# Optimization experiments

Hardware: AMD Instinct MI355X
Metric: run time of the kernel (lower is better)

Reference implementation:

```python
import jax, jax.numpy as jnp
import numpy as np

N, TX, NH, H, E, V = 64, 1024, 512, 512, 300, 32000
IP = NH + H            # attention input size = 1024
HALF = IP // 2         # 512
BN_EPS = 1e-5


def setup_inputs() -> dict:
    key = jax.random.key(0)
    ks = jax.random.split(key, 24)
    p = lambda k, shape: jax.random.normal(k, shape, dtype=jnp.float32) * 0.05
    embed_W = p(ks[0], (V, E)).at[0].set(0.0)  # padding_idx=0 row zeroed
    return {
        "yt_prev": jax.random.randint(ks[1], (N,), 0, V, dtype=jnp.int32),
        "h0": jax.random.normal(ks[2], (N, H), dtype=jnp.float32),
        "c0": jax.random.normal(ks[3], (N, H), dtype=jnp.float32),
        "h1": jax.random.normal(ks[4], (N, H), dtype=jnp.float32),
        "c1": jax.random.normal(ks[5], (N, H), dtype=jnp.float32),
        "encoder_output": jax.random.normal(ks[6], (N, TX, NH), dtype=jnp.float32),
        "c_prev": jax.random.normal(ks[7], (N, NH), dtype=jnp.float32),
        "embed_W": embed_W,
        # pre LSTM cell: input = NH + E
        "pre_W_ih": p(ks[8], (4 * H, NH + E)), "pre_W_hh": p(ks[9], (4 * H, H)),
        "pre_b_ih": p(ks[10], (4 * H,)), "pre_b_hh": p(ks[11], (4 * H,)),
        # post LSTM cell: input = H + NH
        "post_W_ih": p(ks[12], (4 * H, H + NH)), "post_W_hh": p(ks[13], (4 * H, H)),
        "post_b_ih": p(ks[14], (4 * H,)), "post_b_hh": p(ks[15], (4 * H,)),
        # attention MLP
        "att_W1": p(ks[16], (HALF, IP)), "att_b1": p(ks[17], (HALF,)),
        "att_W2": p(ks[18], (1, HALF)), "att_b2": p(ks[19], (1,)),
        # classifier
        "mlp_W": p(ks[20], (V, H)), "mlp_b": p(ks[21], (V,)),
        "bn_gamma": jnp.ones((V,), jnp.float32), "bn_beta": jnp.zeros((V,), jnp.float32),
    }


def _lstm_cell(x, h, c, W_ih, W_hh, b_ih, b_hh):
    # PyTorch LSTMCell gate order: i, f, g, o
    g = x @ W_ih.T + h @ W_hh.T + (b_ih + b_hh)
    i, f, gg, o = jnp.split(g, 4, axis=-1)
    c_new = jax.nn.sigmoid(f) * c + jax.nn.sigmoid(i) * jnp.tanh(gg)
    h_new = jax.nn.sigmoid(o) * jnp.tanh(c_new)
    return h_new, c_new


def reference(yt_prev, h0, c0, h1, c1, encoder_output, c_prev, embed_W,
              pre_W_ih, pre_W_hh, pre_b_ih, pre_b_hh,
              post_W_ih, post_W_hh, post_b_ih, post_b_hh,
              att_W1, att_b1, att_W2, att_b2,
              mlp_W, mlp_b, bn_gamma, bn_beta):
    # embedding lookup + concat with previous context
    y_emb = embed_W[yt_prev]                              # [N, E]
    rnn_input = jnp.concatenate([y_emb, c_prev], axis=1)  # [N, E+NH]
    h_0, c_0 = _lstm_cell(rnn_input, h0, c0, pre_W_ih, pre_W_hh, pre_b_ih, pre_b_hh)
    s_i = h_0
    # Bahdanau attention over encoder timesteps
    Tx = encoder_output.shape[1]
    s_exp = jnp.broadcast_to(s_i[:, None, :], (s_i.shape[0], Tx, s_i.shape[1]))
    concat = jnp.concatenate([encoder_output, s_exp], axis=2)  # [N, Tx, IP]
    e = jax.nn.relu(concat @ att_W1.T + att_b1)                # [N, Tx, HALF]
    scores = e @ att_W2.T + att_b2                             # [N, Tx, 1]
    alphas = jax.nn.softmax(scores, axis=1)                    # softmax over Tx
    context = jnp.sum(alphas * encoder_output, axis=1)         # [N, NH]
    # post LSTM cell
    spell_input = jnp.concatenate([s_i, context], axis=1)
    h_1, c_1 = _lstm_cell(spell_input, h1, c1, post_W_ih, post_W_hh, post_b_ih, post_b_hh)
    # classifier: linear -> relu -> batchnorm(train mode, batch stats) -> softmax
    z = jax.nn.relu(h_1 @ mlp_W.T + mlp_b)                     # [N, V]
    mean = jnp.mean(z, axis=0)
    var = jnp.mean((z - mean) ** 2, axis=0)                    # biased, as in PyTorch training
    z_bn = bn_gamma * (z - mean) * jax.lax.rsqrt(var + BN_EPS) + bn_beta
    out = jax.nn.softmax(z_bn, axis=1)
    return out, h_0, c_0, h_1, c_1, context
```

## Files before the change

### kernel.cpp

```cpp
#include <hip/hip_runtime.h>
#include <math.h>

#define DEVFN __device__ __forceinline__

typedef __attribute__((ext_vector_type(4))) float f32x4;
typedef __attribute__((ext_vector_type(8))) __bf16 bf16x8;
typedef __attribute__((ext_vector_type(8))) short short8v;

#define NB   64
#define TXD  1024
#define NHD  512
#define HSZ  512
#define ESZ  300
#define VSZ  32000
#define G4   (4*HSZ)
#define KPRE (ESZ + NHD + HSZ)
#define KPOST 1536
#define HALFD 512

DEVFN short f2bf(float f) {
  unsigned u = __float_as_uint(f);
  u = (u + 0x7fffu + ((u >> 16) & 1u)) >> 16;
  return (short)u;
}
DEVFN float sigm(float x) { return 1.0f / (1.0f + __expf(-x)); }

DEVFN short8v pack8(float4 a, float4 b) {
  short8v v;
  v[0]=f2bf(a.x); v[1]=f2bf(a.y); v[2]=f2bf(a.z); v[3]=f2bf(a.w);
  v[4]=f2bf(b.x); v[5]=f2bf(b.y); v[6]=f2bf(b.z); v[7]=f2bf(b.w);
  return v;
}
DEVFN void gload16(const void* g, void* lds_base) {
  __builtin_amdgcn_global_load_lds(
      (const __attribute__((address_space(1))) unsigned int*)g,
      (__attribute__((address_space(3))) unsigned int*)lds_base, 16, 0, 0);
}

DEVFN float4 ldA4(const float* __restrict__ A, int lda, int row, int k, int Ka) {
  if (k >= Ka) { float4 z = {0.f,0.f,0.f,0.f}; return z; }
  return *(const float4*)(A + (size_t)row * lda + k);
}
DEVFN float4 ldB4(const float* __restrict__ B1, int ldb1, int split,
                  const float* __restrict__ B2, int ldb2, int row, int k, int Ka) {
  if (k >= Ka) { float4 z = {0.f,0.f,0.f,0.f}; return z; }
  if (k < split) return *(const float4*)(B1 + (size_t)row * ldb1 + k);
  return *(const float4*)(B2 + (size_t)row * ldb2 + (k - split));
}

__global__ __launch_bounds__(256)
void prep(const int* __restrict__ yt, const float* __restrict__ embW,
          const float* __restrict__ c_prev, const float* __restrict__ h0,
          const float* __restrict__ W1, unsigned short* __restrict__ W1b,
          float* __restrict__ cat)
{
  int b = blockIdx.x;
  if (b < 128) {
    int i = b * 256 + threadIdx.x;
    int c = i >> 6, kq = (i & 63) * 8;
    float4 a = *(const float4*)(W1 + (size_t)c * 1024 + kq);
    float4 bb = *(const float4*)(W1 + (size_t)c * 1024 + kq + 4);
    *(short8v*)(W1b + (size_t)c * 512 + kq) = pack8(a, bb);
  } else {
    int i = (b - 128) * 256 + threadIdx.x;
    if (i >= NB * KPRE) return;
    int n = i / KPRE, c = i - n * KPRE;
    float v;
    if (c < ESZ)            v = embW[(size_t)yt[n] * ESZ + c];
    else if (c < ESZ + NHD) v = c_prev[(size_t)n * NHD + (c - ESZ)];
    else                    v = h0[(size_t)n * HSZ + (c - ESZ - NHD)];
    cat[i] = v;
  }
}

template<int EPI>
__global__ __launch_bounds__(256)
void mfma_gemm128(const float* __restrict__ A, int lda, int Ka,
                  const float* __restrict__ B1, int ldb1, int split,
                  const float* __restrict__ B2, int ldb2,
                  const float* __restrict__ bias1,
                  float* __restrict__ C, int ldc, int Kslice,
                  const float* __restrict__ gamma, const float* __restrict__ beta,
                  float* __restrict__ bnsc, float* __restrict__ bnsh)
{
  __shared__ __align__(16) short As[64][40];
  __shared__ __align__(16) short Bs[128][40];
  const int tid = threadIdx.x;
  const int w = tid >> 6, lane = tid & 63;
  const int wr = w >> 1, wc = w & 1;
  const int cl = lane & 15, g = lane >> 4;
  const int n0 = blockIdx.x * 128;
  const int ks = blockIdx.y;
  const int kbeg = ks * Kslice;
  const int kend = min(kbeg + Kslice, Ka);
  C += (size_t)ks * 64 * ldc;

  const f32x4 fz = {0.f,0.f,0.f,0.f};
  f32x4 acc[2][4];
  #pragma unroll
  for (int i = 0; i < 2; ++i)
    #pragma unroll
    for (int j = 0; j < 4; ++j) acc[i][j] = fz;

  const int sr  = tid >> 2;
  const int skc = (tid & 3) * 8;

  float4 ra0, ra1, rb0[2], rb1[2];
  ra0 = ldA4(A, lda, sr, kbeg + skc, Ka);
  ra1 = ldA4(A, lda, sr, kbeg + skc + 4, Ka);
  #pragma unroll
  for (int it = 0; it < 2; ++it) {
    rb0[it] = ldB4(B1, ldb1, split, B2, ldb2, n0 + sr + it*64, kbeg + skc, Ka);
    rb1[it] = ldB4(B1, ldb1, split, B2, ldb2, n0 + sr + it*64, kbeg + skc + 4, Ka);
  }

  for (int k0 = kbeg; k0 < kend; k0 += 32) {
    __syncthreads();
    *(short8v*)&As[sr][skc] = pack8(ra0, ra1);
    #pragma unroll
    for (int it = 0; it < 2; ++it)
      *(short8v*)&Bs[sr + it*64][skc] = pack8(rb0[it], rb1[it]);
    __syncthreads();
    if (k0 + 32 < kend) {
      ra0 = ldA4(A, lda, sr, k0 + 32 + skc, Ka);
      ra1 = ldA4(A, lda, sr, k0 + 32 + skc + 4, Ka);
      #pragma unroll
      for (int it = 0; it < 2; ++it) {
        rb0[it] = ldB4(B1, ldb1, split, B2, ldb2, n0 + sr + it*64, k0 + 32 + skc, Ka);
        rb1[it] = ldB4(B1, ldb1, split, B2, ldb2, n0 + sr + it*64, k0 + 32 + skc + 4, Ka);
      }
    }
    bf16x8 af[2], bfr[4];
    #pragma unroll
    for (int mi = 0; mi < 2; ++mi)
      af[mi] = *(const bf16x8*)&As[wr*32 + mi*16 + cl][g * 8];
    #pragma unroll
    for (int ni = 0; ni < 4; ++ni)
      bfr[ni] = *(const bf16x8*)&Bs[wc*64 + ni*16 + cl][g * 8];
    #pragma unroll
    for (int mi = 0; mi < 2; ++mi)
      #pragma unroll
      for (int ni = 0; ni < 4; ++ni)
        acc[mi][ni] = __builtin_amdgcn_mfma_f32_16x16x32_bf16(af[mi], bfr[ni], acc[mi][ni], 0, 0, 0);
  }

  float s1[4] = {0.f,0.f,0.f,0.f}, s2[4] = {0.f,0.f,0.f,0.f};
  #pragma unroll
  for (int ni = 0; ni < 4; ++ni) {
    int nn = n0 + wc*64 + ni*16 + cl;
    float b = (EPI == 4) ? bias1[nn] : 0.f;
    #pragma unroll
    for (int mi = 0; mi < 2; ++mi)
      #pragma unroll
      for (int r = 0; r < 4; ++r) {
        int m = wr*32 + mi*16 + g*4 + r;
        float v = acc[mi][ni][r];
        if (EPI == 4) v = fmaxf(v + b, 0.f);
        C[(size_t)m * ldc + nn] = v;
        if (EPI == 4) { s1[ni] += v; s2[ni] = fmaf(v, v, s2[ni]); }
      }
  }
  if (EPI == 4) {
    #pragma unroll
    for (int mm = 16; mm < 64; mm <<= 1)
      #pragma unroll
      for (int ni = 0; ni < 4; ++ni) {
        s1[ni] += __shfl_xor(s1[ni], mm, 64);
        s2[ni] += __shfl_xor(s2[ni], mm, 64);
      }
    float* red = (float*)As;
    __syncthreads();
    if (g == 0) {
      #pragma unroll
      for (int ni = 0; ni < 4; ++ni) {
        int col = wc*64 + ni*16 + cl;
        red[(wr*128 + col)*2 + 0] = s1[ni];
        red[(wr*128 + col)*2 + 1] = s2[ni];
      }
    }
    __syncthreads();
    if (tid < 128) {
      int col = n0 + tid;
      float a1 = red[tid*2] + red[(128 + tid)*2];
      float a2 = red[tid*2 + 1] + red[(128 + tid)*2 + 1];
      float mean = a1 * (1.0f / NB);
      float var = a2 * (1.0f / NB) - mean * mean;
      float rr = rsqrtf(var + 1e-5f);
      float sc = gamma[col] * rr;
      bnsc[col] = sc;
      bnsh[col] = beta[col] - mean * sc;
    }
  }
}

__global__ __launch_bounds__(256)
void lstm_point2(const float* __restrict__ gp, int np,
                 const float* __restrict__ bih, const float* __restrict__ bhh,
                 const float* __restrict__ c_old,
                 float* __restrict__ h_new, float* __restrict__ c_new)
{
  int i = blockIdx.x * 256 + threadIdx.x;
  int n = i >> 9, k = i & 511;
  float g[4];
  #pragma unroll
  for (int j = 0; j < 4; ++j) {
    int idx = j * 512 + k;
    float s = bih[idx] + bhh[idx];
    for (int ks = 0; ks < np; ++ks)
      s += gp[((size_t)ks*64 + n) * G4 + idx];
    g[j] = s;
  }
  float c = sigm(g[1]) * c_old[i] + sigm(g[0]) * tanhf(g[2]);
  float h = sigm(g[3]) * tanhf(c);
  h_new[i] = h; c_new[i] = c;
}

__global__ __launch_bounds__(512)
void att_fused(const float* __restrict__ enc, const unsigned short* __restrict__ W1b,
               const float* __restrict__ W2, const float* __restrict__ sprojp,
               const float* __restrict__ b1,
               float* __restrict__ mbuf, float* __restrict__ sbuf,
               float* __restrict__ ctxp)
{
  __shared__ __align__(16) char smem[122880];
  const int tid = threadIdx.x;
  const int wid = tid >> 6, lane = tid & 63;
  const int wr = wid >> 2, wc = wid & 3;
  const int cl = lane & 15, g = lane >> 4;
  const int rt = blockIdx.x;
  const int r0 = rt << 7;
  const int n  = rt >> 3;

  const int a_row = tid >> 2;
  const int a_line = a_row >> 1;
  const int a_waddr = a_line*128 + (a_row & 1)*64 + (((tid & 3) ^ (a_line & 3)) << 4);
  const int b_r = ((lane >> 3) << 1) + ((lane >> 2) & 1);
  const int b_q = (((lane & 3) ^ ((lane >> 3) & 3)) << 3);

  const f32x4 fz = {0.f,0.f,0.f,0.f};
  f32x4 acc[4][8];
  #pragma unroll
  for (int mi = 0; mi < 4; ++mi)
    #pragma unroll
    for (int ni = 0; ni < 8; ++ni) acc[mi][ni] = fz;

  float4 a_lo, a_hi;
  #define A_LOAD(tt) do { \
    const float* asrc = enc + (size_t)(r0 + a_row) * 512 + (tt) * 32 + (tid & 3) * 8; \
    a_lo = *(const float4*)asrc; a_hi = *(const float4*)(asrc + 4); } while (0)
  #define A_WRITE(buf) \
    *(short8v*)(smem + (buf) * 8192 + a_waddr) = pack8(a_lo, a_hi)
  #define STAGE_B(buf, tt) do { int k0 = (tt) * 32; \
    _Pragma("unroll") \
    for (int jj = 0; jj < 4; ++jj) { int j = (wid << 2) + jj; \
      gload16(W1b + (size_t)((j << 4) + b_r) * 512 + k0 + b_q, \
              smem + 24576 + (buf) * 32768 + (j << 10)); } } while (0)

  A_LOAD(0);
  __builtin_amdgcn_sched_barrier(0);
  STAGE_B(0, 0);
  asm volatile("s_waitcnt vmcnt(4)" ::: "memory");
  A_WRITE(0);
  A_LOAD(1);
  __builtin_amdgcn_sched_barrier(0);
  STAGE_B(1, 1);
  asm volatile("s_waitcnt vmcnt(6)" ::: "memory");
  asm volatile("s_waitcnt lgkmcnt(0)" ::: "memory");
  __builtin_amdgcn_s_barrier();
  __builtin_amdgcn_sched_barrier(0);

  for (int t = 0; t < 16; ++t) {
    const int s = t % 3;
    if (t < 15) {
      asm volatile("s_waitcnt vmcnt(4)" ::: "memory");
      A_WRITE((t + 1) % 3);
    }
    if (t < 14) {
      A_LOAD(t + 2);
      __builtin_amdgcn_sched_barrier(0);
      STAGE_B((t + 2) % 3, t + 2);
    }
    const char* Ab = smem + s * 8192;
    const char* Bb = smem + 24576 + s * 32768;
    bf16x8 af[4];
    #pragma unroll
    for (int mi = 0; mi < 4; ++mi) {
      int r = wr * 64 + mi * 16 + cl;
      af[mi] = *(const bf16x8*)(Ab + (r >> 1) * 128 + (r & 1) * 64
                                + ((g ^ ((r >> 1) & 3)) << 4));
    }
    #pragma unroll
    for (int ni = 0; ni < 8; ++ni) {
      int r = wc * 128 + ni * 16 + cl;
      bf16x8 bf = *(const bf16x8*)(Bb + (r >> 1) * 128 + (r & 1) * 64
                                   + ((g ^ ((r >> 1) & 3)) << 4));
      #pragma unroll
      for (int mi = 0; mi < 4; ++mi)
        acc[mi][ni] = __builtin_amdgcn_mfma_f32_16x16x32_bf16(af[mi], bf, acc[mi][ni], 0, 0, 0);
    }
    if (t < 15) {
      if (t < 14) asm volatile("s_waitcnt vmcnt(6)" ::: "memory");
      else        asm volatile("s_waitcnt vmcnt(0)" ::: "memory");
      asm volatile("s_waitcnt lgkmcnt(0)" ::: "memory");
      __builtin_amdgcn_s_barrier();
      __builtin_amdgcn_sched_barrier(0);
    }
  }
  #undef A_LOAD
  #undef A_WRITE
  #undef STAGE_B
  __syncthreads();

  float part[4][4] = {};
  #pragma unroll
  for (int ni = 0; ni < 8; ++ni) {
    int c = wc*128 + ni*16 + cl;
    float spv = b1[c];
    #pragma unroll
    for (int ks = 0; ks < 4; ++ks)
      spv += sprojp[((size_t)ks*64 + n) * HALFD + c];
    float w2 = W2[c];
    #pragma unroll
    for (int mi = 0; mi < 4; ++mi)
      #pragma unroll
      for (int r = 0; r < 4; ++r)
        part[mi][r] += fmaxf(acc[mi][ni][r] + spv, 0.f) * w2;
  }
  #pragma unroll
  for (int mm = 1; mm < 16; mm <<= 1)
    #pragma unroll
    for (int mi = 0; mi < 4; ++mi)
      #pragma unroll
      for (int r = 0; r < 4; ++r)
        part[mi][r] += __shfl_xor(part[mi][r], mm, 64);
  float* red = (float*)smem;
  float* sc  = (float*)(smem + 2048);
  float* eV  = (float*)(smem + 2560);
  if (cl == 0) {
    #pragma unroll
    for (int mi = 0; mi < 4; ++mi)
      #pragma unroll
      for (int r = 0; r < 4; ++r)
        red[wid*64 + mi*16 + g*4 + r] = part[mi][r];
  }
  __syncthreads();
  if (tid < 128) {
    int h = tid >> 6, idx = tid & 63;
    sc[tid] = red[(h*4 + 0)*64 + idx] + red[(h*4 + 1)*64 + idx]
            + red[(h*4 + 2)*64 + idx] + red[(h*4 + 3)*64 + idx];
  }
  __syncthreads();
  if (tid < 64) {
    float s0 = sc[tid], s1v = sc[tid + 64];
    float M = fmaxf(s0, s1v);
    #pragma unroll
    for (int mm = 32; mm >= 1; mm >>= 1) M = fmaxf(M, __shfl_xor(M, mm, 64));
    float e0 = __expf(s0 - M), e1 = __expf(s1v - M);
    eV[tid] = e0; eV[tid + 64] = e1;
    float S = e0 + e1;
    #pragma unroll
    for (int mm = 32; mm >= 1; mm >>= 1) S += __shfl_xor(S, mm, 64);
    if (tid == 0) { mbuf[rt] = M; sbuf[rt] = S; }
  }
  __syncthreads();

  f32x4* red4 = (f32x4*)(smem + 24576);
  {
    const int cgrp = tid & 127, tq = tid >> 7;
    const float* ebase = enc + (size_t)r0 * 512 + (cgrp << 2);
    f32x4 a4 = fz;
    #pragma unroll 8
    for (int tt = 0; tt < 32; ++tt) {
      int t = tq*32 + tt;
      float et = eV[t];
      float4 x = *(const float4*)(ebase + (size_t)t * 512);
      a4[0] = fmaf(et, x.x, a4[0]);
      a4[1] = fmaf(et, x.y, a4[1]);
      a4[2] = fmaf(et, x.z, a4[2]);
      a4[3] = fmaf(et, x.w, a4[3]);
    }
    red4[tq*128 + cgrp] = a4;
  }
  __syncthreads();
  if (tid < 128) {
    f32x4 s4 = red4[tid];
    f32x4 b4 = red4[128 + tid];
    f32x4 c4 = red4[256 + tid];
    f32x4 d4 = red4[384 + tid];
    f32x4 o4;
    #pragma unroll
    for (int i = 0; i < 4; ++i) o4[i] = s4[i] + b4[i] + c4[i] + d4[i];
    *(f32x4*)(ctxp + (size_t)rt * 512 + tid*4) = o4;
  }
}

__global__ __launch_bounds__(256)
void att_combine(const float* __restrict__ mbuf, const float* __restrict__ sbuf,
                 const float* __restrict__ ctxp, const float* __restrict__ h0out,
                 const float* __restrict__ h1in,
                 float* __restrict__ ctx_out, float* __restrict__ cat)
{
  int i = blockIdx.x * 256 + threadIdx.x;
  int n = i >> 9, c = i & 511;
  float M = -1e30f;
  #pragma unroll
  for (int b = 0; b < 8; ++b) M = fmaxf(M, mbuf[n*8 + b]);
  float S = 0.f, ctx = 0.f;
  #pragma unroll
  for (int b = 0; b < 8; ++b) {
    float w = __expf(mbuf[n*8 + b] - M);
    S = fmaf(sbuf[n*8 + b], w, S);
    ctx = fmaf(ctxp[(size_t)(n*8 + b)*512 + c], w, ctx);
  }
  ctx /= S;
  ctx_out[i] = ctx;
  cat[(size_t)n * KPOST + c] = h0out[i];
  cat[(size_t)n * KPOST + HSZ + c] = ctx;
  cat[(size_t)n * KPOST + 2*HSZ + c] = h1in[i];
}

__global__ __launch_bounds__(1024)
void softmax_v(const float* __restrict__ z, const float* __restrict__ scale,
               const float* __restrict__ shift, float* __restrict__ out)
{
  int n = blockIdx.x, tid = threadIdx.x;
  const float* zr = z + (size_t)n * VSZ;
  float* orow = out + (size_t)n * VSZ;
  __shared__ float rb[16];
  __shared__ float sb[16];
  float v[32]; float mx = -1e30f;
  #pragma unroll
  for (int i = 0; i < 32; ++i) {
    int j = tid + i*1024;
    v[i] = (j < VSZ) ? fmaf(zr[j], scale[j], shift[j]) : -1e30f;
    mx = fmaxf(mx, v[i]);
  }
  #pragma unroll
  for (int m = 32; m >= 1; m >>= 1) mx = fmaxf(mx, __shfl_xor(mx, m, 64));
  if ((tid & 63) == 0) rb[tid >> 6] = mx;
  __syncthreads();
  #pragma unroll
  for (int i = 0; i < 16; ++i) mx = fmaxf(mx, rb[i]);
  float s = 0.f;
  #pragma unroll
  for (int i = 0; i < 32; ++i) { v[i] = __expf(v[i] - mx); s += v[i]; }
  #pragma unroll
  for (int m = 32; m >= 1; m >>= 1) s += __shfl_xor(s, m, 64);
  if ((tid & 63) == 0) sb[tid >> 6] = s;
  __syncthreads();
  s = 0.f;
  #pragma unroll
  for (int i = 0; i < 16; ++i) s += sb[i];
  float inv = 1.0f / s;
  #pragma unroll
  for (int i = 0; i < 32; ++i) {
    int j = tid + i*1024;
    if (j < VSZ) orow[j] = v[i] * inv;
  }
}

extern "C" void kernel_launch(void* const* d_in, const int* in_sizes, int n_in,
                              void* d_out, int out_size, void* d_ws, size_t ws_size,
                              hipStream_t stream)
{
  const int*   yt       = (const int*)  d_in[0];
  const float* h0       = (const float*)d_in[1];
  const float* c0       = (const float*)d_in[2];
  const float* h1       = (const float*)d_in[3];
  const float* c1       = (const float*)d_in[4];
  const float* enc      = (const float*)d_in[5];
  const float* c_prev   = (const float*)d_in[6];
  const float* embW     = (const float*)d_in[7];
  const float* pre_Wih  = (const float*)d_in[8];
  const float* pre_Whh  = (const float*)d_in[9];
  const float* pre_bih  = (const float*)d_in[10];
  const float* pre_bhh  = (const float*)d_in[11];
  const float* post_Wih = (const float*)d_in[12];
  const float* post_Whh = (const float*)d_in[13];
  const float* post_bih = (const float*)d_in[14];
  const float* post_bhh = (const float*)d_in[15];
  const float* att_W1   = (const float*)d_in[16];
  const float* att_b1   = (const float*)d_in[17];
  const float* att_W2   = (const float*)d_in[18];
  const float* mlp_W    = (const float*)d_in[20];
  const float* mlp_b    = (const float*)d_in[21];
  const float* bn_g     = (const float*)d_in[22];
  const float* bn_b     = (const float*)d_in[23];

  float* out   = (float*)d_out;
  float* o_h0  = out + (size_t)NB * VSZ;
  float* o_c0  = o_h0 + NB * HSZ;
  float* o_h1  = o_c0 + NB * HSZ;
  float* o_c1  = o_h1 + NB * HSZ;
  float* o_ctx = o_c1 + NB * HSZ;

  float* ws = (float*)d_ws;
  float* pre_cat  = ws;
  float* gatesp   = ws + 84736;
  float* sprojp   = ws + 1264384;
  float* mbuf     = ws + 1395456;
  float* sbuf     = ws + 1396480;
  float* ctxp     = ws + 1397504;
  float* post_cat = ws + 1921792;
  unsigned short* W1b = (unsigned short*)(ws + 2020096);
  float* zbuf     = ws;
  float* bnsc     = ws + 2151168;
  float* bnsh     = ws + 2183168;

  prep<<<459, 256, 0, stream>>>(yt, embW, c_prev, h0, att_W1, W1b, pre_cat);
  mfma_gemm128<0><<<dim3(G4/128, 9), 256, 0, stream>>>(
      pre_cat, KPRE, KPRE, pre_Wih, ESZ + NHD, ESZ + NHD, pre_Whh, HSZ,
      nullptr, gatesp, G4, 160, nullptr, nullptr, nullptr, nullptr);
  lstm_point2<<<NB*HSZ/256, 256, 0, stream>>>(gatesp, 9, pre_bih, pre_bhh, c0, o_h0, o_c0);
  mfma_gemm128<0><<<dim3(HALFD/128, 4), 256, 0, stream>>>(
      o_h0, HSZ, HSZ, att_W1 + NHD, NHD + HSZ, HSZ, att_W1 + NHD, NHD + HSZ,
      nullptr, sprojp, HALFD, 128, nullptr, nullptr, nullptr, nullptr);
  att_fused<<<512, 512, 0, stream>>>(enc, W1b, att_W2, sprojp, att_b1,
                                     mbuf, sbuf, ctxp);
  att_combine<<<NB*NHD/256, 256, 0, stream>>>(mbuf, sbuf, ctxp, o_h0, h1, o_ctx, post_cat);
  mfma_gemm128<0><<<dim3(G4/128, 8), 256, 0, stream>>>(
      post_cat, KPOST, KPOST, post_Wih, HSZ + NHD, HSZ + NHD, post_Whh, HSZ,
      nullptr, gatesp, G4, 192, nullptr, nullptr, nullptr, nullptr);
  lstm_point2<<<NB*HSZ/256, 256, 0, stream>>>(gatesp, 8, post_bih, post_bhh, c1, o_h1, o_c1);
  mfma_gemm128<4><<<dim3(VSZ/128, 1), 256, 0, stream>>>(
      o_h1, HSZ, HSZ, mlp_W, HSZ, HSZ, mlp_W, HSZ, mlp_b, zbuf, VSZ, 512,
      bn_g, bn_b, bnsc, bnsh);
  softmax_v<<<NB, 1024, 0, stream>>>(zbuf, bnsc, bnsh, out);
}
```

Before: 143.9 us.

## Double the attention GEMM K-tile and split the vocab softmax across more blocks

Two independent changes. The attention kernel's K tile grows from 32 to 64, with a two-stage double buffer replacing the three-stage ring and a swizzle over 8 lanes instead of 4. This halves the number of loop iterations and barriers, but shared memory rises to 160KB. Separately, the 64-block row softmax becomes a two-pass split over 4 chunks of 8000 (256 blocks) to raise parallelism; the second pass re-reads z and recomputes exp rather than keeping values in registers.

```diff
diff --git a/kernel.cpp b/kernel.cpp
--- a/kernel.cpp
+++ b/kernel.cpp
@@ -222,7 +222,7 @@
                float* __restrict__ mbuf, float* __restrict__ sbuf,
                float* __restrict__ ctxp)
 {
-  __shared__ __align__(16) char smem[122880];
+  __shared__ __align__(16) char smem[163840];
   const int tid = threadIdx.x;
   const int wid = tid >> 6, lane = tid & 63;
   const int wr = wid >> 2, wc = wid & 3;
@@ -231,11 +231,12 @@
   const int r0 = rt << 7;
   const int n  = rt >> 3;
 
-  const int a_row = tid >> 2;
-  const int a_line = a_row >> 1;
-  const int a_waddr = a_line*128 + (a_row & 1)*64 + (((tid & 3) ^ (a_line & 3)) << 4);
-  const int b_r = ((lane >> 3) << 1) + ((lane >> 2) & 1);
-  const int b_q = (((lane & 3) ^ ((lane >> 3) & 3)) << 3);
+  const int a_row = tid >> 2, a_q = tid & 3;
+  const float* a_src = enc + (size_t)(r0 + a_row) * 512 + a_q * 16;
+  const int a_w0 = a_row*128 + ((((a_q<<1)  ) ^ (a_row & 7)) << 4);
+  const int a_w1 = a_row*128 + ((((a_q<<1)|1) ^ (a_row & 7)) << 4);
+  const int b_rl = lane >> 3, b_s = lane & 7;
+  const int b_k = (b_s ^ b_rl) << 3;
 
   const f32x4 fz = {0.f,0.f,0.f,0.f};
   f32x4 acc[4][8];
@@ -244,63 +245,67 @@
     #pragma unroll
     for (int ni = 0; ni < 8; ++ni) acc[mi][ni] = fz;
 
-  float4 a_lo, a_hi;
-  #define A_LOAD(tt) do { \
-    const float* asrc = enc + (size_t)(r0 + a_row) * 512 + (tt) * 32 + (tid & 3) * 8; \
-    a_lo = *(const float4*)asrc; a_hi = *(const float4*)(asrc + 4); } while (0)
-  #define A_WRITE(buf) \
-    *(short8v*)(smem + (buf) * 8192 + a_waddr) = pack8(a_lo, a_hi)
-  #define STAGE_B(buf, tt) do { int k0 = (tt) * 32; \
+  float4 av0, av1, av2, av3;
+  #define A_LOAD(tt) do { const float* p = a_src + (tt) * 64; \
+    av0 = *(const float4*)(p);      av1 = *(const float4*)(p + 4); \
+    av2 = *(const float4*)(p + 8);  av3 = *(const float4*)(p + 12); } while (0)
+  #define A_WRITE(buf) do { \
+    *(short8v*)(smem + (buf) * 16384 + a_w0) = pack8(av0, av1); \
+    *(short8v*)(smem + (buf) * 16384 + a_w1) = pack8(av2, av3); } while (0)
+  #define STAGE_B(buf, tt) do { int k0 = (tt) * 64; \
     _Pragma("unroll") \
-    for (int jj = 0; jj < 4; ++jj) { int j = (wid << 2) + jj; \
-      gload16(W1b + (size_t)((j << 4) + b_r) * 512 + k0 + b_q, \
-              smem + 24576 + (buf) * 32768 + (j << 10)); } } while (0)
+    for (int jj = 0; jj < 8; ++jj) { \
+      int row = (wid << 6) + (jj << 3) + b_rl; \
+      gload16(W1b + (size_t)row * 512 + k0 + b_k, \
+              smem + 32768 + (buf) * 65536 + (wid << 13) + (jj << 10)); } } while (0)
 
   A_LOAD(0);
   __builtin_amdgcn_sched_barrier(0);
+  asm volatile("s_waitcnt vmcnt(0)" ::: "memory");
+  A_WRITE(0);
   STAGE_B(0, 0);
-  asm volatile("s_waitcnt vmcnt(4)" ::: "memory");
-  A_WRITE(0);
+  __builtin_amdgcn_sched_barrier(0);
   A_LOAD(1);
   __builtin_amdgcn_sched_barrier(0);
-  STAGE_B(1, 1);
-  asm volatile("s_waitcnt vmcnt(6)" ::: "memory");
+  asm volatile("s_waitcnt vmcnt(4)" ::: "memory");
   asm volatile("s_waitcnt lgkmcnt(0)" ::: "memory");
   __builtin_amdgcn_s_barrier();
   __builtin_amdgcn_sched_barrier(0);
 
-  for (int t = 0; t < 16; ++t) {
-    const int s = t % 3;
-    if (t < 15) {
-      asm volatile("s_waitcnt vmcnt(4)" ::: "memory");
-      A_WRITE((t + 1) % 3);
-    }
-    if (t < 14) {
-      A_LOAD(t + 2);
+  for (int t = 0; t < 8; ++t) {
+    const int s = t & 1;
+    if (t < 7) {
+      asm volatile("s_waitcnt vmcnt(0)" ::: "memory");
+      A_WRITE(s ^ 1);
+      STAGE_B(s ^ 1, t + 1);
       __builtin_amdgcn_sched_barrier(0);
-      STAGE_B((t + 2) % 3, t + 2);
-    }
-    const char* Ab = smem + s * 8192;
-    const char* Bb = smem + 24576 + s * 32768;
-    bf16x8 af[4];
-    #pragma unroll
-    for (int mi = 0; mi < 4; ++mi) {
-      int r = wr * 64 + mi * 16 + cl;
-      af[mi] = *(const bf16x8*)(Ab + (r >> 1) * 128 + (r & 1) * 64
-                                + ((g ^ ((r >> 1) & 3)) << 4));
-    }
-    #pragma unroll
-    for (int ni = 0; ni < 8; ++ni) {
-      int r = wc * 128 + ni * 16 + cl;
-      bf16x8 bf = *(const bf16x8*)(Bb + (r >> 1) * 128 + (r & 1) * 64
-                                   + ((g ^ ((r >> 1) & 3)) << 4));
-      #pragma unroll
-      for (int mi = 0; mi < 4; ++mi)
-        acc[mi][ni] = __builtin_amdgcn_mfma_f32_16x16x32_bf16(af[mi], bf, acc[mi][ni], 0, 0, 0);
-    }
-    if (t < 15) {
-      if (t < 14) asm volatile("s_waitcnt vmcnt(6)" ::: "memory");
-      else        asm volatile("s_waitcnt vmcnt(0)" ::: "memory");
+      if (t < 6) {
+        A_LOAD(t + 2);
+        __builtin_amdgcn_sched_barrier(0);
+      }
+    }
+    const char* Ab = smem + s * 16384;
+    const char* Bb = smem + 32768 + s * 65536;
+    #pragma unroll
+    for (int kk = 0; kk < 2; ++kk) {
+      bf16x8 af[4];
+      #pragma unroll
+      for (int mi = 0; mi < 4; ++mi) {
+        int r = wr * 64 + mi * 16 + cl;
+        af[mi] = *(const bf16x8*)(Ab + r * 128 + ((((kk<<2)+g) ^ (r & 7)) << 4));
+      }
+      #pragma unroll
+      for (int ni = 0; ni < 8; ++ni) {
+        int r = wc * 128 + ni * 16 + cl;
+        bf16x8 bf = *(const bf16x8*)(Bb + r * 128 + ((((kk<<2)+g) ^ (r & 7)) << 4));
+        #pragma unroll
+        for (int mi = 0; mi < 4; ++mi)
+          acc[mi][ni] = __builtin_amdgcn_mfma_f32_16x16x32_bf16(af[mi], bf, acc[mi][ni], 0, 0, 0);
+      }
+    }
+    if (t < 7) {
+      if (t < 6) asm volatile("s_waitcnt vmcnt(4)" ::: "memory");
+      else       asm volatile("s_waitcnt vmcnt(0)" ::: "memory");
       asm volatile("s_waitcnt lgkmcnt(0)" ::: "memory");
       __builtin_amdgcn_s_barrier();
       __builtin_amdgcn_sched_barrier(0);
@@ -364,7 +369,7 @@
   }
   __syncthreads();
 
-  f32x4* red4 = (f32x4*)(smem + 24576);
+  f32x4* red4 = (f32x4*)(smem + 32768);
   {
     const int cgrp = tid & 127, tq = tid >> 7;
     const float* ebase = enc + (size_t)r0 * 512 + (cgrp << 2);
@@ -419,43 +424,65 @@
   cat[(size_t)n * KPOST + 2*HSZ + c] = h1in[i];
 }
 
-__global__ __launch_bounds__(1024)
-void softmax_v(const float* __restrict__ z, const float* __restrict__ scale,
-               const float* __restrict__ shift, float* __restrict__ out)
-{
-  int n = blockIdx.x, tid = threadIdx.x;
+__global__ __launch_bounds__(256)
+void smv_part(const float* __restrict__ z, const float* __restrict__ scale,
+              const float* __restrict__ shift,
+              float* __restrict__ pm, float* __restrict__ ps)
+{
+  int vq = blockIdx.x, n = blockIdx.y, tid = threadIdx.x;
+  int base = vq * 8000;
   const float* zr = z + (size_t)n * VSZ;
-  float* orow = out + (size_t)n * VSZ;
-  __shared__ float rb[16];
-  __shared__ float sb[16];
+  __shared__ float rb[4], sb[4];
   float v[32]; float mx = -1e30f;
   #pragma unroll
   for (int i = 0; i < 32; ++i) {
-    int j = tid + i*1024;
-    v[i] = (j < VSZ) ? fmaf(zr[j], scale[j], shift[j]) : -1e30f;
+    int o = tid + i*256;
+    int j = base + o;
+    v[i] = (o < 8000) ? fmaf(zr[j], scale[j], shift[j]) : -1e30f;
     mx = fmaxf(mx, v[i]);
   }
   #pragma unroll
   for (int m = 32; m >= 1; m >>= 1) mx = fmaxf(mx, __shfl_xor(mx, m, 64));
   if ((tid & 63) == 0) rb[tid >> 6] = mx;
   __syncthreads();
-  #pragma unroll
-  for (int i = 0; i < 16; ++i) mx = fmaxf(mx, rb[i]);
+  mx = fmaxf(fmaxf(rb[0], rb[1]), fmaxf(rb[2], rb[3]));
   float s = 0.f;
   #pragma unroll
-  for (int i = 0; i < 32; ++i) { v[i] = __expf(v[i] - mx); s += v[i]; }
+  for (int i = 0; i < 32; ++i) {
+    int o = tid + i*256;
+    if (o < 8000) s += __expf(v[i] - mx);
+  }
   #pragma unroll
   for (int m = 32; m >= 1; m >>= 1) s += __shfl_xor(s, m, 64);
   if ((tid & 63) == 0) sb[tid >> 6] = s;
   __syncthreads();
-  s = 0.f;
-  #pragma unroll
-  for (int i = 0; i < 16; ++i) s += sb[i];
-  float inv = 1.0f / s;
+  if (tid == 0) {
+    pm[n*4 + vq] = mx;
+    ps[n*4 + vq] = sb[0] + sb[1] + sb[2] + sb[3];
+  }
+}
+
+__global__ __launch_bounds__(256)
+void smv_final(const float* __restrict__ z, const float* __restrict__ scale,
+               const float* __restrict__ shift,
+               const float* __restrict__ pm, const float* __restrict__ ps,
+               float* __restrict__ out)
+{
+  int vq = blockIdx.x, n = blockIdx.y, tid = threadIdx.x;
+  int base = vq * 8000;
+  const float* zr = z + (size_t)n * VSZ;
+  float M = fmaxf(fmaxf(pm[n*4], pm[n*4+1]), fmaxf(pm[n*4+2], pm[n*4+3]));
+  float S = 0.f;
+  #pragma unroll
+  for (int k = 0; k < 4; ++k) S = fmaf(ps[n*4+k], __expf(pm[n*4+k] - M), S);
+  float inv = 1.0f / S;
   #pragma unroll
   for (int i = 0; i < 32; ++i) {
-    int j = tid + i*1024;
-    if (j < VSZ) orow[j] = v[i] * inv;
+    int o = tid + i*256;
+    if (o < 8000) {
+      int j = base + o;
+      out[(size_t)n * VSZ + j] = __expf(fmaf(zr[j], scale[j], shift[j]) - M) * inv;
+    }
   }
 }
 
@@ -506,6 +533,8 @@
   float* zbuf     = ws;
   float* bnsc     = ws + 2151168;
   float* bnsh     = ws + 2183168;
+  float* pm       = ws + 2215168;
+  float* psb      = ws + 2215424;
 
   prep<<<459, 256, 0, stream>>>(yt, embW, c_prev, h0, att_W1, W1b, pre_cat);
   mfma_gemm128<0><<<dim3(G4/128, 9), 256, 0, stream>>>(
@@ -525,5 +554,6 @@
   mfma_gemm128<4><<<dim3(VSZ/128, 1), 256, 0, stream>>>(
       o_h1, HSZ, HSZ, mlp_W, HSZ, HSZ, mlp_W, HSZ, mlp_b, zbuf, VSZ, 512,
       bn_g, bn_b, bnsc, bnsh);
-  softmax_v<<<NB, 1024, 0, stream>>>(zbuf, bnsc, bnsh, out);
-}
+  smv_part<<<dim3(4, NB), 256, 0, stream>>>(zbuf, bnsc, bnsh, pm, psb);
+  smv_final<<<dim3(4, NB), 256, 0, stream>>>(zbuf, bnsc, bnsh, pm, psb, out);
+}
```

New measurement: 144.3 us. No clear change (+0.3%).
